# Kernel tuning notes

Measured on AMD Instinct MI355X. Metric: run time of the kernel, lower is better.

The kernel has to match this reference:

```python
import jax, jax.numpy as jnp
import numpy as np

T, B, E, H = 2048, 2, 1024, 16
HD = E // H

def setup_inputs() -> dict:
    key = jax.random.key(0)
    k1, k2, k3 = jax.random.split(key, 3)
    x = jax.random.normal(k1, (T, B, E), dtype=jnp.float32)
    # xavier-uniform-like scale for weights
    in_proj_w = jax.random.normal(k2, (3 * E, E), dtype=jnp.float32) * (2.0 / (4 * E)) ** 0.5
    in_proj_b = jnp.zeros((3 * E,), dtype=jnp.float32)
    out_w = jax.random.normal(k3, (E, E), dtype=jnp.float32) * (1.0 / E) ** 0.5
    out_b = jnp.zeros((E,), dtype=jnp.float32)
    return {"x": x, "in_proj_w": in_proj_w, "in_proj_b": in_proj_b, "out_w": out_w, "out_b": out_b}

def reference(x, in_proj_w, in_proj_b, out_w, out_b):
    t, b, e = x.shape
    scale = HD ** (-0.5)
    # fused QKV projection: F.linear(x, W, b) = x @ W.T + b
    qkv = x @ in_proj_w.T + in_proj_b            # [T, B, 3E]
    q, k, v = jnp.split(qkv, 3, axis=-1)         # each [T, B, E]
    q = q * scale
    # reshape to heads: [T, B, E] -> [B, H, T, HD]
    def to_heads(a):
        return a.reshape(t, b, H, HD).transpose(1, 2, 0, 3)
    qh, kh, vh = to_heads(q), to_heads(k), to_heads(v)
    # scores [B, H, T, T] -- full NxN materialization, same as torch.bmm
    scores = jnp.einsum('bhtd,bhsd->bhts', qh, kh)
    w = jax.nn.softmax(scores.astype(jnp.float32), axis=-1).astype(scores.dtype)
    attn = jnp.einsum('bhts,bhsd->bhtd', w, vh)  # [B, H, T, HD]
    attn = attn.transpose(2, 0, 1, 3).reshape(t, b, e)  # [T, B, E]
    attn = attn @ out_w.T + out_b
    attn_weights = w.sum(axis=1) / H             # [B, T, T] head-averaged
    return attn, attn_weights
```

## Files before the change

kernel.cpp:

```cpp
#include <hip/hip_runtime.h>
#include <hip/hip_bf16.h>
#include <cstdint>

#define T_DIM 2048
#define B_DIM 2
#define E_DIM 1024
#define H_DIM 16
#define HD_DIM 64
#define M_DIM 4096
#define N1_DIM 3072
#define QK_SCALE 0.125f

typedef __attribute__((ext_vector_type(8))) short bfrag;
typedef __attribute__((ext_vector_type(4))) float f32x4;

__device__ __forceinline__ short f2bf(float f) {
  union { float f; uint32_t u; } v; v.f = f;
  uint32_t r = v.u + 0x7fffu + ((v.u >> 16) & 1u);
  return (short)(r >> 16);
}
__device__ __forceinline__ float bf2f(short b) {
  union { uint32_t u; float f; } v; v.u = ((uint32_t)(uint16_t)b) << 16;
  return v.f;
}
__device__ __forceinline__ f32x4 mfma16(bfrag a, bfrag b, f32x4 c) {
  return __builtin_amdgcn_mfma_f32_16x16x32_bf16(a, b, c, 0, 0, 0);
}

__global__ void split_kernel(const float* __restrict__ in,
                             short* __restrict__ hi, short* __restrict__ lo, int n) {
  int i = blockIdx.x * blockDim.x + threadIdx.x;
  int stride = gridDim.x * blockDim.x;
  for (; i < n; i += stride) {
    float v = in[i];
    short h = f2bf(v);
    hi[i] = h;
    lo[i] = f2bf(v - bf2f(h));
  }
}

template<int N_T, int K_T, bool OUT_BF16, bool DO_SCALE>
__global__ __launch_bounds__(256) void gemm_split(
    const short* __restrict__ Ahi, const short* __restrict__ Alo,
    const short* __restrict__ Bhi, const short* __restrict__ Blo,
    const float* __restrict__ bias, void* __restrict__ Cout)
{
  constexpr int BK = 32;
  constexpr int LDT = BK + 8;
  __shared__ short As[2][128][LDT];
  __shared__ short Bs[2][128][LDT];

  const int m0 = blockIdx.y * 128;
  const int n0 = blockIdx.x * 128;
  const int tid = threadIdx.x;
  const int lane = tid & 63;
  const int wave = tid >> 6;
  const int wr = (wave >> 1) * 64;
  const int wc = (wave & 1) * 64;

  f32x4 acc[4][4];
#pragma unroll
  for (int i = 0; i < 4; ++i)
#pragma unroll
    for (int j = 0; j < 4; ++j) acc[i][j] = f32x4{0.f, 0.f, 0.f, 0.f};

  const int ldr = tid >> 1;
  const int ldc0 = (tid & 1) << 4;

  for (int k0 = 0; k0 < K_T; k0 += BK) {
    const size_t aoff = (size_t)(m0 + ldr) * K_T + k0 + ldc0;
    const size_t boff = (size_t)(n0 + ldr) * K_T + k0 + ldc0;
    bfrag ah0 = *(const bfrag*)(Ahi + aoff);
    bfrag ah1 = *(const bfrag*)(Ahi + aoff + 8);
    bfrag al0 = *(const bfrag*)(Alo + aoff);
    bfrag al1 = *(const bfrag*)(Alo + aoff + 8);
    bfrag bh0 = *(const bfrag*)(Bhi + boff);
    bfrag bh1 = *(const bfrag*)(Bhi + boff + 8);
    bfrag bl0 = *(const bfrag*)(Blo + boff);
    bfrag bl1 = *(const bfrag*)(Blo + boff + 8);
    __syncthreads();
    *(bfrag*)&As[0][ldr][ldc0]     = ah0;
    *(bfrag*)&As[0][ldr][ldc0 + 8] = ah1;
    *(bfrag*)&As[1][ldr][ldc0]     = al0;
    *(bfrag*)&As[1][ldr][ldc0 + 8] = al1;
    *(bfrag*)&Bs[0][ldr][ldc0]     = bh0;
    *(bfrag*)&Bs[0][ldr][ldc0 + 8] = bh1;
    *(bfrag*)&Bs[1][ldr][ldc0]     = bl0;
    *(bfrag*)&Bs[1][ldr][ldc0 + 8] = bl1;
    __syncthreads();

    const int fr = lane & 15;
    const int fk = (lane >> 4) << 3;
    bfrag afh[4], afl[4];
#pragma unroll
    for (int fi = 0; fi < 4; ++fi) {
      afh[fi] = *(const bfrag*)&As[0][wr + fi * 16 + fr][fk];
      afl[fi] = *(const bfrag*)&As[1][wr + fi * 16 + fr][fk];
    }
#pragma unroll
    for (int fj = 0; fj < 4; ++fj) {
      bfrag bfh = *(const bfrag*)&Bs[0][wc + fj * 16 + fr][fk];
      bfrag bfl = *(const bfrag*)&Bs[1][wc + fj * 16 + fr][fk];
#pragma unroll
      for (int fi = 0; fi < 4; ++fi) {
        acc[fi][fj] = mfma16(afh[fi], bfh, acc[fi][fj]);
        acc[fi][fj] = mfma16(afh[fi], bfl, acc[fi][fj]);
        acc[fi][fj] = mfma16(afl[fi], bfh, acc[fi][fj]);
      }
    }
  }

  const int cr = (lane >> 4) << 2;
  const int cc = lane & 15;
#pragma unroll
  for (int fi = 0; fi < 4; ++fi)
#pragma unroll
    for (int fj = 0; fj < 4; ++fj)
#pragma unroll
      for (int r = 0; r < 4; ++r) {
        int m = m0 + wr + fi * 16 + cr + r;
        int n = n0 + wc + fj * 16 + cc;
        float v = acc[fi][fj][r] + bias[n];
        if (DO_SCALE) { if (n < E_DIM) v *= QK_SCALE; }
        if (OUT_BF16) ((short*)Cout)[(size_t)m * N_T + n] = f2bf(v);
        else          ((float*)Cout)[(size_t)m * N_T + n] = v;
      }
}

__global__ __launch_bounds__(256) void attn_kernel(
    const short* __restrict__ qkv,
    float* __restrict__ linv_ws,
    short* __restrict__ ctx_hi, short* __restrict__ ctx_lo)
{
  __shared__ short Ks[2][64][72];
  __shared__ short Vt[2][64][72];
  __shared__ short Ps[128][76];

  const int bh = blockIdx.x;
  const int b  = bh >> 4;
  const int h  = bh & 15;
  const int t0 = blockIdx.y * 128;
  const int tid  = threadIdx.x;
  const int lane = tid & 63;
  const int wave = tid >> 6;
  const int fr = lane & 15;
  const int fk = (lane >> 4) << 3;
  const int cr = (lane >> 4) << 2;

  bfrag aq[2][2];
#pragma unroll
  for (int hh = 0; hh < 2; ++hh) {
    const size_t qb = ((size_t)(t0 + 32 * wave + 16 * hh + fr) * B_DIM + b) * N1_DIM + h * HD_DIM;
    aq[hh][0] = *(const bfrag*)(qkv + qb + fk);
    aq[hh][1] = *(const bfrag*)(qkv + qb + fk + 32);
  }

  bfrag ones;
#pragma unroll
  for (int j = 0; j < 8; ++j) ones[j] = (short)0x3F80;

  f32x4 pv[2][4];
  f32x4 pvsum[2];
#pragma unroll
  for (int hh = 0; hh < 2; ++hh) {
    pvsum[hh] = f32x4{0.f, 0.f, 0.f, 0.f};
#pragma unroll
    for (int fd = 0; fd < 4; ++fd) pv[hh][fd] = f32x4{0.f, 0.f, 0.f, 0.f};
  }

  const int r  = tid >> 2;
  const int ds = (tid & 3) << 4;
  const int vc0 = (((r >> 3) ^ (ds >> 3)) << 3) | (r & 7);
  const int vc1 = (((r >> 3) ^ ((ds >> 3) + 1)) << 3) | (r & 7);

  constexpr int NT = T_DIM / 64;
  const size_t kstep = ((size_t)64 * B_DIM) * N1_DIM;
  size_t kb = ((size_t)r * B_DIM + b) * N1_DIM + E_DIM + h * HD_DIM + ds;

  bfrag kv0 = *(const bfrag*)(qkv + kb);
  bfrag kv1 = *(const bfrag*)(qkv + kb + 8);
  bfrag vv0 = *(const bfrag*)(qkv + kb + E_DIM);
  bfrag vv1 = *(const bfrag*)(qkv + kb + E_DIM + 8);
  *(bfrag*)&Ks[0][r][ds]     = kv0;
  *(bfrag*)&Ks[0][r][ds + 8] = kv1;
#pragma unroll
  for (int j = 0; j < 8; ++j) Vt[0][ds + j][vc0]     = vv0[j];
#pragma unroll
  for (int j = 0; j < 8; ++j) Vt[0][ds + 8 + j][vc1] = vv1[j];
  kb += kstep;
  kv0 = *(const bfrag*)(qkv + kb);
  kv1 = *(const bfrag*)(qkv + kb + 8);
  vv0 = *(const bfrag*)(qkv + kb + E_DIM);
  vv1 = *(const bfrag*)(qkv + kb + E_DIM + 8);

  for (int st = 0; st < NT; ++st) {
    const int p = st & 1;
    __syncthreads();

    f32x4 sacc[2][4];
    __builtin_amdgcn_s_setprio(1);
#pragma unroll
    for (int fs = 0; fs < 4; ++fs) {
      bfrag bk0 = *(const bfrag*)&Ks[p][fs * 16 + fr][fk];
      bfrag bk1 = *(const bfrag*)&Ks[p][fs * 16 + fr][fk + 32];
#pragma unroll
      for (int hh = 0; hh < 2; ++hh) {
        f32x4 a = f32x4{0.f, 0.f, 0.f, 0.f};
        a = mfma16(aq[hh][0], bk0, a);
        a = mfma16(aq[hh][1], bk1, a);
        sacc[hh][fs] = a;
      }
    }
    __builtin_amdgcn_s_setprio(0);

    if (st + 1 < NT) {
      *(bfrag*)&Ks[p ^ 1][r][ds]     = kv0;
      *(bfrag*)&Ks[p ^ 1][r][ds + 8] = kv1;
#pragma unroll
      for (int j = 0; j < 8; ++j) Vt[p ^ 1][ds + j][vc0]     = vv0[j];
#pragma unroll
      for (int j = 0; j < 8; ++j) Vt[p ^ 1][ds + 8 + j][vc1] = vv1[j];
    }
    if (st + 2 < NT) {
      kb += kstep;
      kv0 = *(const bfrag*)(qkv + kb);
      kv1 = *(const bfrag*)(qkv + kb + 8);
      vv0 = *(const bfrag*)(qkv + kb + E_DIM);
      vv1 = *(const bfrag*)(qkv + kb + E_DIM + 8);
    }

#pragma unroll
    for (int hh = 0; hh < 2; ++hh) {
#pragma unroll
      for (int fs = 0; fs < 4; ++fs)
#pragma unroll
        for (int rr = 0; rr < 4; ++rr)
          Ps[32 * wave + 16 * hh + cr + rr][fs * 16 + fr] = f2bf(__expf(sacc[hh][fs][rr]));

      bfrag pa0 = *(const bfrag*)&Ps[32 * wave + 16 * hh + fr][fk];
      bfrag pa1 = *(const bfrag*)&Ps[32 * wave + 16 * hh + fr][fk + 32];
      pvsum[hh] = mfma16(pa0, ones, pvsum[hh]);
      pvsum[hh] = mfma16(pa1, ones, pvsum[hh]);
      __builtin_amdgcn_s_setprio(1);
#pragma unroll
      for (int fd = 0; fd < 4; ++fd) {
        const int R = fd * 16 + fr;
        const int sg = (R >> 3) & 7;
        bfrag bv0 = *(const bfrag*)&Vt[p][R][(((fk >> 3) ^ sg) << 3)];
        bfrag bv1 = *(const bfrag*)&Vt[p][R][((((fk >> 3) + 4) ^ sg) << 3)];
        pv[hh][fd] = mfma16(pa0, bv0, pv[hh][fd]);
        pv[hh][fd] = mfma16(pa1, bv1, pv[hh][fd]);
      }
      __builtin_amdgcn_s_setprio(0);
    }
  }

#pragma unroll
  for (int hh = 0; hh < 2; ++hh)
#pragma unroll
    for (int rr = 0; rr < 4; ++rr) {
      const int row = 32 * wave + 16 * hh + cr + rr;
      const float inv = 1.0f / pvsum[hh][rr];
      if (fr == 0) linv_ws[(size_t)bh * T_DIM + t0 + row] = inv;
#pragma unroll
      for (int fd = 0; fd < 4; ++fd) {
        float v = pv[hh][fd][rr] * inv;
        int d = fd * 16 + fr;
        size_t off = ((size_t)(t0 + row) * B_DIM + b) * E_DIM + h * HD_DIM + d;
        short hi = f2bf(v);
        ctx_hi[off] = hi;
        ctx_lo[off] = f2bf(v - bf2f(hi));
      }
    }
}

__global__ __launch_bounds__(256) void weights_kernel(
    const short* __restrict__ qkv, const float* __restrict__ linv,
    float* __restrict__ outw)
{
  __shared__ short Qs[64][72];
  __shared__ short Ks[64][72];
  __shared__ float Ls[16][64];

  const int s0 = blockIdx.x * 64;
  const int bt = blockIdx.y;
  const int b  = bt >> 5;
  const int t0 = (bt & 31) * 64;
  const int tid  = threadIdx.x;
  const int lane = tid & 63;
  const int wave = tid >> 6;
  const int fr = lane & 15;
  const int fk = (lane >> 4) << 3;
  const int cr = (lane >> 4) << 2;

  {
    const int h  = tid >> 4;
    const int r4 = (tid & 15) << 2;
    float4 v = *(const float4*)(linv + (size_t)(b * H_DIM + h) * T_DIM + t0 + r4);
    Ls[h][r4 + 0] = v.x * (1.0f / H_DIM);
    Ls[h][r4 + 1] = v.y * (1.0f / H_DIM);
    Ls[h][r4 + 2] = v.z * (1.0f / H_DIM);
    Ls[h][r4 + 3] = v.w * (1.0f / H_DIM);
  }

  f32x4 wacc[4];
#pragma unroll
  for (int i = 0; i < 4; ++i) wacc[i] = f32x4{0.f, 0.f, 0.f, 0.f};

  const int r  = tid >> 2;
  const int ds = (tid & 3) << 4;

  for (int h = 0; h < H_DIM; ++h) {
    const size_t qbase = ((size_t)(t0 + r) * B_DIM + b) * N1_DIM + h * HD_DIM + ds;
    const size_t kbase = ((size_t)(s0 + r) * B_DIM + b) * N1_DIM + E_DIM + h * HD_DIM + ds;
    bfrag q0 = *(const bfrag*)(qkv + qbase);
    bfrag q1 = *(const bfrag*)(qkv + qbase + 8);
    bfrag k0 = *(const bfrag*)(qkv + kbase);
    bfrag k1 = *(const bfrag*)(qkv + kbase + 8);
    __syncthreads();
    *(bfrag*)&Qs[r][ds]     = q0;
    *(bfrag*)&Qs[r][ds + 8] = q1;
    *(bfrag*)&Ks[r][ds]     = k0;
    *(bfrag*)&Ks[r][ds + 8] = k1;
    __syncthreads();

    bfrag aq0 = *(const bfrag*)&Qs[wave * 16 + fr][fk];
    bfrag aq1 = *(const bfrag*)&Qs[wave * 16 + fr][fk + 32];
#pragma unroll
    for (int fs = 0; fs < 4; ++fs) {
      bfrag bk0 = *(const bfrag*)&Ks[fs * 16 + fr][fk];
      bfrag bk1 = *(const bfrag*)&Ks[fs * 16 + fr][fk + 32];
      f32x4 a = f32x4{0.f, 0.f, 0.f, 0.f};
      a = mfma16(aq0, bk0, a);
      a = mfma16(aq1, bk1, a);
#pragma unroll
      for (int rr = 0; rr < 4; ++rr)
        wacc[fs][rr] += __expf(a[rr]) * Ls[h][wave * 16 + cr + rr];
    }
  }

#pragma unroll
  for (int fs = 0; fs < 4; ++fs)
#pragma unroll
    for (int rr = 0; rr < 4; ++rr) {
      const int t = t0 + wave * 16 + cr + rr;
      outw[((size_t)b * T_DIM + t) * T_DIM + s0 + fs * 16 + fr] = wacc[fs][rr];
    }
}

extern "C" void kernel_launch(void* const* d_in, const int* in_sizes, int n_in,
                              void* d_out, int out_size, void* d_ws, size_t ws_size,
                              hipStream_t stream) {
  const float* x  = (const float*)d_in[0];
  const float* w1 = (const float*)d_in[1];
  const float* b1 = (const float*)d_in[2];
  const float* w2 = (const float*)d_in[3];
  const float* b2 = (const float*)d_in[4];
  float* out = (float*)d_out;

  char* ws = (char*)d_ws;
  size_t off = 0;
  auto carve = [&](size_t bytes) -> void* {
    void* p = ws + off;
    off = (off + bytes + 255) & ~(size_t)255;
    return p;
  };
  short* x_hi  = (short*)carve((size_t)M_DIM * E_DIM * 2);
  short* x_lo  = (short*)carve((size_t)M_DIM * E_DIM * 2);
  short* w1_hi = (short*)carve((size_t)N1_DIM * E_DIM * 2);
  short* w1_lo = (short*)carve((size_t)N1_DIM * E_DIM * 2);
  short* w2_hi = (short*)carve((size_t)E_DIM * E_DIM * 2);
  short* w2_lo = (short*)carve((size_t)E_DIM * E_DIM * 2);
  short* qkv   = (short*)carve((size_t)M_DIM * N1_DIM * 2);
  float* linv  = (float*)carve((size_t)B_DIM * H_DIM * T_DIM * 4);
  short* c_hi  = (short*)carve((size_t)M_DIM * E_DIM * 2);
  short* c_lo  = (short*)carve((size_t)M_DIM * E_DIM * 2);

  split_kernel<<<2048, 256, 0, stream>>>(x,  x_hi,  x_lo,  M_DIM * E_DIM);
  split_kernel<<<2048, 256, 0, stream>>>(w1, w1_hi, w1_lo, N1_DIM * E_DIM);
  split_kernel<<<1024, 256, 0, stream>>>(w2, w2_hi, w2_lo, E_DIM * E_DIM);

  gemm_split<N1_DIM, E_DIM, true, true><<<dim3(N1_DIM / 128, M_DIM / 128), 256, 0, stream>>>(
      x_hi, x_lo, w1_hi, w1_lo, b1, (void*)qkv);

  attn_kernel<<<dim3(B_DIM * H_DIM, T_DIM / 128), 256, 0, stream>>>(
      qkv, linv, c_hi, c_lo);

  weights_kernel<<<dim3(T_DIM / 64, B_DIM * (T_DIM / 64)), 256, 0, stream>>>(
      qkv, linv, out + (size_t)M_DIM * E_DIM);

  gemm_split<E_DIM, E_DIM, false, false><<<dim3(E_DIM / 128, M_DIM / 128), 256, 0, stream>>>(
      c_hi, c_lo, w2_hi, w2_lo, b2, (void*)out);
}
```

Baseline: 339.8 us.

## Fuse split kernels, use direct global-to-LDS loads in GEMM, pipeline weights kernel

The three fp32-to-bf16 hi/lo split launches become one vectorized kernel that handles four elements per thread. The split GEMM now stages tiles with global_load_lds (direct global-to-LDS DMA) instead of going through registers, and drops the LDS row padding, which may add bank conflicts on the fragment reads. The weights kernel keeps Q fragments in registers, double-buffers K in LDS with register prefetch two heads ahead, and cuts one barrier per head. These target launch overhead, memory latency and synchronization cost across several kernels.

Result: slower. 391.4 us (+15.2%).

```diff
diff --git a/kernel.cpp b/kernel.cpp
--- a/kernel.cpp
+++ b/kernel.cpp
@@ -12,6 +12,7 @@
 #define QK_SCALE 0.125f
 
 typedef __attribute__((ext_vector_type(8))) short bfrag;
+typedef __attribute__((ext_vector_type(4))) short short4v;
 typedef __attribute__((ext_vector_type(4))) float f32x4;
 
 __device__ __forceinline__ short f2bf(float f) {
@@ -26,16 +27,41 @@
 __device__ __forceinline__ f32x4 mfma16(bfrag a, bfrag b, f32x4 c) {
   return __builtin_amdgcn_mfma_f32_16x16x32_bf16(a, b, c, 0, 0, 0);
 }
-
-__global__ void split_kernel(const float* __restrict__ in,
-                             short* __restrict__ hi, short* __restrict__ lo, int n) {
-  int i = blockIdx.x * blockDim.x + threadIdx.x;
-  int stride = gridDim.x * blockDim.x;
-  for (; i < n; i += stride) {
-    float v = in[i];
-    short h = f2bf(v);
-    hi[i] = h;
-    lo[i] = f2bf(v - bf2f(h));
+__device__ __forceinline__ void gload16(const short* g, short* l) {
+  __builtin_amdgcn_global_load_lds(
+      (const __attribute__((address_space(1))) unsigned int*)g,
+      (__attribute__((address_space(3))) unsigned int*)l, 16, 0, 0);
+}
+
+__global__ void split3_kernel(
+    const float* __restrict__ x,  const float* __restrict__ w1, const float* __restrict__ w2,
+    short* __restrict__ xh,  short* __restrict__ xl,
+    short* __restrict__ w1h, short* __restrict__ w1l,
+    short* __restrict__ w2h, short* __restrict__ w2l)
+{
+  constexpr int NA = M_DIM * E_DIM;
+  constexpr int NB = N1_DIM * E_DIM;
+  constexpr int NC = E_DIM * E_DIM;
+  constexpr int TOT4 = (NA + NB + NC) >> 2;
+  int t = blockIdx.x * blockDim.x + threadIdx.x;
+  const int stride = gridDim.x * blockDim.x;
+  for (; t < TOT4; t += stride) {
+    int i = t << 2;
+    const float* s; short* dh; short* dl;
+    if (i < NA)            { s = x;  dh = xh;  dl = xl; }
+    else if (i < NA + NB)  { i -= NA;       s = w1; dh = w1h; dl = w1l; }
+    else                   { i -= NA + NB;  s = w2; dh = w2h; dl = w2l; }
+    float4 v = *(const float4*)(s + i);
+    short4v h, l;
+    float vv[4] = {v.x, v.y, v.z, v.w};
+#pragma unroll
+    for (int c = 0; c < 4; ++c) {
+      short hb = f2bf(vv[c]);
+      h[c] = hb;
+      l[c] = f2bf(vv[c] - bf2f(hb));
+    }
+    *(short4v*)(dh + i) = h;
+    *(short4v*)(dl + i) = l;
   }
 }
 
@@ -45,10 +71,8 @@
     const short* __restrict__ Bhi, const short* __restrict__ Blo,
     const float* __restrict__ bias, void* __restrict__ Cout)
 {
-  constexpr int BK = 32;
-  constexpr int LDT = BK + 8;
-  __shared__ short As[2][128][LDT];
-  __shared__ short Bs[2][128][LDT];
+  __shared__ short As[2][128][32];
+  __shared__ short Bs[2][128][32];
 
   const int m0 = blockIdx.y * 128;
   const int n0 = blockIdx.x * 128;
@@ -64,33 +88,25 @@
 #pragma unroll
     for (int j = 0; j < 4; ++j) acc[i][j] = f32x4{0.f, 0.f, 0.f, 0.f};
 
-  const int ldr = tid >> 1;
-  const int ldc0 = (tid & 1) << 4;
-
-  for (int k0 = 0; k0 < K_T; k0 += BK) {
-    const size_t aoff = (size_t)(m0 + ldr) * K_T + k0 + ldc0;
-    const size_t boff = (size_t)(n0 + ldr) * K_T + k0 + ldc0;
-    bfrag ah0 = *(const bfrag*)(Ahi + aoff);
-    bfrag ah1 = *(const bfrag*)(Ahi + aoff + 8);
-    bfrag al0 = *(const bfrag*)(Alo + aoff);
-    bfrag al1 = *(const bfrag*)(Alo + aoff + 8);
-    bfrag bh0 = *(const bfrag*)(Bhi + boff);
-    bfrag bh1 = *(const bfrag*)(Bhi + boff + 8);
-    bfrag bl0 = *(const bfrag*)(Blo + boff);
-    bfrag bl1 = *(const bfrag*)(Blo + boff + 8);
+  const int srow = (wave << 5) + (lane >> 2);
+  const int scol = (lane & 3) << 3;
+  const int fr = lane & 15;
+  const int fk = (lane >> 4) << 3;
+
+  for (int k0 = 0; k0 < K_T; k0 += 32) {
+    const size_t abase = (size_t)(m0 + srow) * K_T + k0 + scol;
+    const size_t bbase = (size_t)(n0 + srow) * K_T + k0 + scol;
     __syncthreads();
-    *(bfrag*)&As[0][ldr][ldc0]     = ah0;
-    *(bfrag*)&As[0][ldr][ldc0 + 8] = ah1;
-    *(bfrag*)&As[1][ldr][ldc0]     = al0;
-    *(bfrag*)&As[1][ldr][ldc0 + 8] = al1;
-    *(bfrag*)&Bs[0][ldr][ldc0]     = bh0;
-    *(bfrag*)&Bs[0][ldr][ldc0 + 8] = bh1;
-    *(bfrag*)&Bs[1][ldr][ldc0]     = bl0;
-    *(bfrag*)&Bs[1][ldr][ldc0 + 8] = bl1;
+    gload16(Ahi + abase,                    &As[0][(wave << 5)][0]);
+    gload16(Ahi + abase + (size_t)16 * K_T, &As[0][(wave << 5) + 16][0]);
+    gload16(Alo + abase,                    &As[1][(wave << 5)][0]);
+    gload16(Alo + abase + (size_t)16 * K_T, &As[1][(wave << 5) + 16][0]);
+    gload16(Bhi + bbase,                    &Bs[0][(wave << 5)][0]);
+    gload16(Bhi + bbase + (size_t)16 * K_T, &Bs[0][(wave << 5) + 16][0]);
+    gload16(Blo + bbase,                    &Bs[1][(wave << 5)][0]);
+    gload16(Blo + bbase + (size_t)16 * K_T, &Bs[1][(wave << 5) + 16][0]);
     __syncthreads();
 
-    const int fr = lane & 15;
-    const int fk = (lane >> 4) << 3;
     bfrag afh[4], afl[4];
 #pragma unroll
     for (int fi = 0; fi < 4; ++fi) {
@@ -278,8 +294,7 @@
     const short* __restrict__ qkv, const float* __restrict__ linv,
     float* __restrict__ outw)
 {
-  __shared__ short Qs[64][72];
-  __shared__ short Ks[64][72];
+  __shared__ short Ks[2][64][72];
   __shared__ float Ls[16][64];
 
   const int s0 = blockIdx.x * 64;
@@ -294,49 +309,70 @@
   const int cr = (lane >> 4) << 2;
 
   {
-    const int h  = tid >> 4;
+    const int hh = tid >> 4;
     const int r4 = (tid & 15) << 2;
-    float4 v = *(const float4*)(linv + (size_t)(b * H_DIM + h) * T_DIM + t0 + r4);
-    Ls[h][r4 + 0] = v.x * (1.0f / H_DIM);
-    Ls[h][r4 + 1] = v.y * (1.0f / H_DIM);
-    Ls[h][r4 + 2] = v.z * (1.0f / H_DIM);
-    Ls[h][r4 + 3] = v.w * (1.0f / H_DIM);
-  }
-
-  f32x4 wacc[4];
-#pragma unroll
-  for (int i = 0; i < 4; ++i) wacc[i] = f32x4{0.f, 0.f, 0.f, 0.f};
+    float4 v = *(const float4*)(linv + (size_t)(b * H_DIM + hh) * T_DIM + t0 + r4);
+    Ls[hh][r4 + 0] = v.x * (1.0f / H_DIM);
+    Ls[hh][r4 + 1] = v.y * (1.0f / H_DIM);
+    Ls[hh][r4 + 2] = v.z * (1.0f / H_DIM);
+    Ls[hh][r4 + 3] = v.w * (1.0f / H_DIM);
+  }
 
   const int r  = tid >> 2;
   const int ds = (tid & 3) << 4;
+  const size_t kb0 = ((size_t)(s0 + r) * B_DIM + b) * N1_DIM + E_DIM + ds;
+  const size_t qb0 = ((size_t)(t0 + wave * 16 + fr) * B_DIM + b) * N1_DIM;
+
+  {
+    bfrag a0 = *(const bfrag*)(qkv + kb0);
+    bfrag a1 = *(const bfrag*)(qkv + kb0 + 8);
+    *(bfrag*)&Ks[0][r][ds]     = a0;
+    *(bfrag*)&Ks[0][r][ds + 8] = a1;
+  }
+  bfrag kna = *(const bfrag*)(qkv + kb0 + HD_DIM);
+  bfrag knb = *(const bfrag*)(qkv + kb0 + HD_DIM + 8);
+  bfrag aq0 = *(const bfrag*)(qkv + qb0 + fk);
+  bfrag aq1 = *(const bfrag*)(qkv + qb0 + fk + 32);
+
+  f32x4 wacc[4];
+#pragma unroll
+  for (int i = 0; i < 4; ++i) wacc[i] = f32x4{0.f, 0.f, 0.f, 0.f};
 
   for (int h = 0; h < H_DIM; ++h) {
-    const size_t qbase = ((size_t)(t0 + r) * B_DIM + b) * N1_DIM + h * HD_DIM + ds;
-    const size_t kbase = ((size_t)(s0 + r) * B_DIM + b) * N1_DIM + E_DIM + h * HD_DIM + ds;
-    bfrag q0 = *(const bfrag*)(qkv + qbase);
-    bfrag q1 = *(const bfrag*)(qkv + qbase + 8);
-    bfrag k0 = *(const bfrag*)(qkv + kbase);
-    bfrag k1 = *(const bfrag*)(qkv + kbase + 8);
+    const int p = h & 1;
     __syncthreads();
-    *(bfrag*)&Qs[r][ds]     = q0;
-    *(bfrag*)&Qs[r][ds + 8] = q1;
-    *(bfrag*)&Ks[r][ds]     = k0;
-    *(bfrag*)&Ks[r][ds + 8] = k1;
-    __syncthreads();
-
-    bfrag aq0 = *(const bfrag*)&Qs[wave * 16 + fr][fk];
-    bfrag aq1 = *(const bfrag*)&Qs[wave * 16 + fr][fk + 32];
+
+    f32x4 sacc[4];
+    __builtin_amdgcn_s_setprio(1);
 #pragma unroll
     for (int fs = 0; fs < 4; ++fs) {
-      bfrag bk0 = *(const bfrag*)&Ks[fs * 16 + fr][fk];
-      bfrag bk1 = *(const bfrag*)&Ks[fs * 16 + fr][fk + 32];
+      bfrag bk0 = *(const bfrag*)&Ks[p][fs * 16 + fr][fk];
+      bfrag bk1 = *(const bfrag*)&Ks[p][fs * 16 + fr][fk + 32];
       f32x4 a = f32x4{0.f, 0.f, 0.f, 0.f};
       a = mfma16(aq0, bk0, a);
       a = mfma16(aq1, bk1, a);
+      sacc[fs] = a;
+    }
+    __builtin_amdgcn_s_setprio(0);
+
+    if (h + 1 < H_DIM) {
+      *(bfrag*)&Ks[p ^ 1][r][ds]     = kna;
+      *(bfrag*)&Ks[p ^ 1][r][ds + 8] = knb;
+    }
+    if (h + 2 < H_DIM) {
+      kna = *(const bfrag*)(qkv + kb0 + (size_t)(h + 2) * HD_DIM);
+      knb = *(const bfrag*)(qkv + kb0 + (size_t)(h + 2) * HD_DIM + 8);
+    }
+    if (h + 1 < H_DIM) {
+      aq0 = *(const bfrag*)(qkv + qb0 + (size_t)(h + 1) * HD_DIM + fk);
+      aq1 = *(const bfrag*)(qkv + qb0 + (size_t)(h + 1) * HD_DIM + fk + 32);
+    }
+
+#pragma unroll
+    for (int fs = 0; fs < 4; ++fs)
 #pragma unroll
       for (int rr = 0; rr < 4; ++rr)
-        wacc[fs][rr] += __expf(a[rr]) * Ls[h][wave * 16 + cr + rr];
-    }
+        wacc[fs][rr] += __expf(sacc[fs][rr]) * Ls[h][wave * 16 + cr + rr];
   }
 
 #pragma unroll
@@ -376,9 +412,7 @@
   short* c_hi  = (short*)carve((size_t)M_DIM * E_DIM * 2);
   short* c_lo  = (short*)carve((size_t)M_DIM * E_DIM * 2);
 
-  split_kernel<<<2048, 256, 0, stream>>>(x,  x_hi,  x_lo,  M_DIM * E_DIM);
-  split_kernel<<<2048, 256, 0, stream>>>(w1, w1_hi, w1_lo, N1_DIM * E_DIM);
-  split_kernel<<<1024, 256, 0, stream>>>(w2, w2_hi, w2_lo, E_DIM * E_DIM);
+  split3_kernel<<<2048, 256, 0, stream>>>(x, w1, w2, x_hi, x_lo, w1_hi, w1_lo, w2_hi, w2_lo);
 
   gemm_split<N1_DIM, E_DIM, true, true><<<dim3(N1_DIM / 128, M_DIM / 128), 256, 0, stream>>>(
       x_hi, x_lo, w1_hi, w1_lo, b1, (void*)qkv);
```
